# Kernel optimization log

Hardware: AMD Instinct MI355X
Metric: run time of the kernel (lower is better)

## Reference

```python
import jax, jax.numpy as jnp
import numpy as np

B, G = 256, 24
N = B * G
D_IN, HEADS, D_HEAD = 128, 8, 64  # out_channels = in_channels//2 = 64, concat=False
EFF = HEADS * D_HEAD
EPS = 1e-5
SCALE = float(np.sqrt(D_HEAD))

def _gelu(x):
    return jax.nn.gelu(x, approximate=False)

def _pff(x, w1, b1, w2, b2):
    # PositionwiseFeedForward, dropout=0 (eval)
    return _gelu(x @ w1.T + b1) @ w2.T + b2

def _graph_norm_global(x, w, b, ms):
    # GraphNorm called without batch -> single graph over all N nodes
    mean = jnp.mean(x, axis=0, keepdims=True)
    out = x - mean * ms
    var = jnp.mean(out * out, axis=0, keepdims=True)
    return w * out / jnp.sqrt(var + EPS) + b

def _graph_norm(x, w, b, ms, batch, nseg):
    cnt = jax.ops.segment_sum(jnp.ones((x.shape[0],), x.dtype), batch, nseg)[:, None]
    mean = jax.ops.segment_sum(x, batch, nseg) / cnt
    out = x - mean[batch] * ms
    var = jax.ops.segment_sum(out * out, batch, nseg) / cnt
    return w * out / jnp.sqrt(var + EPS)[batch] + b

def _segment_softmax(logits, seg, nseg):
    m = jax.ops.segment_max(logits, seg, num_segments=nseg)
    e = jnp.exp(logits - m[seg])
    s = jax.ops.segment_sum(e, seg, num_segments=nseg)
    return e / (s[seg] + 1e-16)

def _attn_conv(x, edge_index, p):
    (nq_w, nq_b, nq_ms, wq, bq, wk, bk, wv, bv,
     no_w, no_b, no_ms, o_w1, o_b1, o_w2, o_b2) = p
    n = x.shape[0]
    xin = x
    xn = _graph_norm_global(x, nq_w, nq_b, nq_ms)
    q = (xn @ wq.T + bq).reshape(n, HEADS, D_HEAD)
    k = (xn @ wk.T + bk).reshape(n, HEADS, D_HEAD)
    v = (xn @ wv.T + bv).reshape(n, HEADS, D_HEAD)
    loops = jnp.arange(n, dtype=edge_index.dtype)  # add_self_loops appends
    src = jnp.concatenate([edge_index[0], loops])
    dst = jnp.concatenate([edge_index[1], loops])
    qk = jnp.sum(q[dst] * k[src], axis=-1) / SCALE          # [E', H]
    alpha = _segment_softmax(qk, dst, n)                     # segment softmax over dst
    aggr = jax.ops.segment_sum(v[src] * alpha[:, :, None], dst, num_segments=n)  # [N,H,Dh]
    aggr = aggr.mean(axis=1)                                 # concat=False: head mean -> [N,64]
    init = xin.reshape(n, D_IN // D_HEAD, D_HEAD).sum(axis=1)  # sum-fold 128 -> 64 residual
    h = aggr + init
    hn = _graph_norm_global(h, no_w, no_b, no_ms)
    return h + _pff(hn, o_w1, o_b1, o_w2, o_b2)


def setup_inputs() -> dict:
    key = jax.random.key(0)
    ks = jax.random.split(key, 12)
    # block-dense edges: fully connected within each set, no self loops
    a = np.arange(G)
    ii, jj = np.meshgrid(a, a, indexing='ij')
    m = ii != jj
    dst_l, src_l = ii[m], jj[m]
    offs = (np.arange(B) * G)[:, None]
    src = (src_l[None, :] + offs).reshape(-1)
    dst = (dst_l[None, :] + offs).reshape(-1)
    edge_index = jnp.asarray(np.stack([src, dst]), dtype=jnp.int64)
    batch = jnp.asarray(np.repeat(np.arange(B), G), dtype=jnp.int64)
    ptr = jnp.asarray(np.arange(B + 1) * G, dtype=jnp.int64)
    x = jax.random.normal(ks[0], (N, D_IN), jnp.float32)
    def lin(k, o, i):
        return jax.random.normal(k, (o, i), jnp.float32) * (1.0 / np.sqrt(i))
    d = dict(x=x, edge_index=edge_index, ptr=ptr, batch=batch)
    d.update(nq_w=jnp.ones((D_IN,)), nq_b=jnp.zeros((D_IN,)), nq_ms=jnp.ones((D_IN,)))
    d.update(wq=lin(ks[1], EFF, D_IN), bq=jnp.zeros((EFF,)),
             wk=lin(ks[2], EFF, D_IN), bk=jnp.zeros((EFF,)),
             wv=lin(ks[3], EFF, D_IN), bv=jnp.zeros((EFF,)))
    d.update(no_w=jnp.ones((D_HEAD,)), no_b=jnp.zeros((D_HEAD,)), no_ms=jnp.ones((D_HEAD,)))
    d.update(o_w1=lin(ks[4], D_HEAD, D_HEAD), o_b1=jnp.zeros((D_HEAD,)),
             o_w2=lin(ks[5], D_HEAD, D_HEAD), o_b2=jnp.zeros((D_HEAD,)))
    d.update(pn_w=jnp.ones((D_HEAD,)), pn_b=jnp.zeros((D_HEAD,)), pn_ms=jnp.ones((D_HEAD,)))
    d.update(p_w1=lin(ks[6], D_HEAD, D_HEAD), p_b1=jnp.zeros((D_HEAD,)),
             p_w2=lin(ks[7], 1, D_HEAD), p_b2=jnp.zeros((1,)))
    return d


def reference(x, edge_index, ptr, batch,
              nq_w, nq_b, nq_ms, wq, bq, wk, bk, wv, bv,
              no_w, no_b, no_ms, o_w1, o_b1, o_w2, o_b2,
              pn_w, pn_b, pn_ms, p_w1, p_b1, p_w2, p_b2):
    nseg = ptr.shape[0] - 1
    h = _attn_conv(x, edge_index,
                   (nq_w, nq_b, nq_ms, wq, bq, wk, bk, wv, bv,
                    no_w, no_b, no_ms, o_w1, o_b1, o_w2, o_b2))   # [N,64]
    hn = _graph_norm(h, pn_w, pn_b, pn_ms, batch, nseg)
    score = _pff(hn, p_w1, p_b1, p_w2, p_b2)                       # [N,1]
    w = _segment_softmax(score[:, 0], batch, nseg)[:, None]        # per-set softmax
    return jax.ops.segment_sum(x * w, batch, num_segments=nseg)    # [B, 128]
```

## Files before the change

kernel.cpp:

```cpp
#include <hip/hip_runtime.h>
#include <stdint.h>


#define N_NODES 6144
#define GSIZE 24
#define NGRAPH 256
#define DIN 128
#define DH 64
#define EFF 512
#define EPSN 1e-5f

typedef __attribute__((ext_vector_type(8))) __bf16 bf16x8;
typedef __attribute__((ext_vector_type(4))) float f32x4;
union U16B { uint4 u; bf16x8 v; unsigned short s[8]; };

__device__ inline unsigned short f2bf(float f){
  unsigned u = __float_as_uint(f);
  u += 0x7fff + ((u>>16)&1);
  return (unsigned short)(u>>16);
}
__device__ inline float gelu_exact(float x){ return 0.5f*x*(1.0f+erff(x*0.70710678118654752f)); }

#define XS    0
#define HS    256
#define WT1   81920
#define WT2   86016
#define PWT1  90112
#define FBo   94208
#define WCVT_BYTE  385024
#define HCOMB_BYTE 778240

#define QSTRIDE 516

__global__ __launch_bounds__(256)
void k_pre(const float* __restrict__ x,
           const float* __restrict__ o_w1, const float* __restrict__ o_w2,
           const float* __restrict__ p_w1,
           const float* __restrict__ o_b1, const float* __restrict__ o_b2,
           const float* __restrict__ p_b1, const float* __restrict__ p_w2,
           const float* __restrict__ p_b2,
           const float* __restrict__ wq, const float* __restrict__ wk,
           const float* __restrict__ wv,
           float* __restrict__ wsf){
  int t = threadIdx.x;
  int bi = blockIdx.x;
  if(bi < 192){
    int c = t & 127, h = t >> 7;
    float s = 0.f, q = 0.f;
    #pragma unroll
    for(int r = 0; r < 16; ++r){
      float v = x[(size_t)(bi*32 + h + 2*r)*DIN + c];
      s += v; q += v*v;
    }
    __shared__ float sm[256], sm2[256];
    sm[t] = s; sm2[t] = q;
    __syncthreads();
    if(t < 128){
      atomicAdd(&wsf[XS + t],       sm[t] + sm[t+128]);
      atomicAdd(&wsf[XS + 128 + t], sm2[t] + sm2[t+128]);
    }
    return;
  }
  if(bi < 195){
    const float* src; float* dst;
    if(bi == 192){ src = o_w1; dst = wsf + WT1; }
    else if(bi == 193){ src = o_w2; dst = wsf + WT2; }
    else { src = p_w1; dst = wsf + PWT1; }
    for(int p = t; p < DH*DH; p += 256){
      int r = p >> 6, c = p & 63;
      dst[c*DH + r] = src[p];
    }
    if(bi == 192){
      float* fb = wsf + FBo;
      if(t < 64){
        fb[t]       = o_b1[t];
        fb[64 + t]  = o_b2[t];
        fb[128 + t] = p_b1[t];
        fb[192 + t] = p_w2[t];
      }
      if(t == 0) fb[256] = p_b2[0];
    }
    return;
  }
  int j = bi - 195;
  int mat = j >> 2, seg = j & 3;
  const float* src = (mat==0) ? wq : (mat==1) ? wk : wv;
  unsigned short* dst = (unsigned short*)((char*)wsf + WCVT_BYTE)
                        + (size_t)mat*EFF*DIN + seg*16384;
  const float* sp = src + seg*16384;
  for(int e = t*8; e < 16384; e += 2048){
    float4 a = *(const float4*)(sp + e);
    float4 b = *(const float4*)(sp + e + 4);
    U16B o;
    o.s[0]=f2bf(a.x); o.s[1]=f2bf(a.y); o.s[2]=f2bf(a.z); o.s[3]=f2bf(a.w);
    o.s[4]=f2bf(b.x); o.s[5]=f2bf(b.y); o.s[6]=f2bf(b.z); o.s[7]=f2bf(b.w);
    *(uint4*)(dst + e) = o.u;
  }
}

#define LOADW(nt, W, B) do{ \
  const int mat_ = (nt)>>2, sub_ = (nt)&3; \
  const unsigned short* wp_ = wcvt + (size_t)mat_*EFF*DIN \
      + (size_t)(h*64 + sub_*16 + m)*DIN + lq*8; \
  W[0] = *(const uint4*)(wp_);      W[1] = *(const uint4*)(wp_ + 32); \
  W[2] = *(const uint4*)(wp_ + 64); W[3] = *(const uint4*)(wp_ + 96); \
  const float* bias_ = (mat_==0) ? bq : (mat_==1) ? bk : bv; \
  B = *(const float4*)(bias_ + h*64 + sub_*16 + lq*4); \
}while(0)

#define COMPW(nt, W, B) do{ \
  const int mat_ = (nt)>>2, sub_ = (nt)&3; \
  f32x4 a0_ = {0.f,0.f,0.f,0.f}, a1_ = {0.f,0.f,0.f,0.f}; \
  U16B w8_; \
  w8_.u = W[0]; \
  a0_ = __builtin_amdgcn_mfma_f32_16x16x32_bf16(w8_.v, afr[0][0], a0_, 0, 0, 0); \
  a1_ = __builtin_amdgcn_mfma_f32_16x16x32_bf16(w8_.v, afr[1][0], a1_, 0, 0, 0); \
  w8_.u = W[1]; \
  a0_ = __builtin_amdgcn_mfma_f32_16x16x32_bf16(w8_.v, afr[0][1], a0_, 0, 0, 0); \
  a1_ = __builtin_amdgcn_mfma_f32_16x16x32_bf16(w8_.v, afr[1][1], a1_, 0, 0, 0); \
  w8_.u = W[2]; \
  a0_ = __builtin_amdgcn_mfma_f32_16x16x32_bf16(w8_.v, afr[0][2], a0_, 0, 0, 0); \
  a1_ = __builtin_amdgcn_mfma_f32_16x16x32_bf16(w8_.v, afr[1][2], a1_, 0, 0, 0); \
  w8_.u = W[3]; \
  a0_ = __builtin_amdgcn_mfma_f32_16x16x32_bf16(w8_.v, afr[0][3], a0_, 0, 0, 0); \
  a1_ = __builtin_amdgcn_mfma_f32_16x16x32_bf16(w8_.v, afr[1][3], a1_, 0, 0, 0); \
  float* dst_ = qlds + mat_*(GSIZE*QSTRIDE); \
  const int col_ = h*64 + sub_*16 + lq*4; \
  { float4 o_; o_.x=a0_[0]+B.x; o_.y=a0_[1]+B.y; o_.z=a0_[2]+B.z; o_.w=a0_[3]+B.w; \
    *(float4*)(dst_ + m*QSTRIDE + col_) = o_; } \
  if(m < 8){ float4 o_; o_.x=a1_[0]+B.x; o_.y=a1_[1]+B.y; o_.z=a1_[2]+B.z; o_.w=a1_[3]+B.w; \
    *(float4*)(dst_ + (16+m)*QSTRIDE + col_) = o_; } \
}while(0)

__global__ __launch_bounds__(512)
void k_attn2(const float* __restrict__ x,
             const float* __restrict__ bq, const float* __restrict__ bk,
             const float* __restrict__ bv,
             const float* __restrict__ nq_w, const float* __restrict__ nq_b,
             const float* __restrict__ nq_ms,
             float* __restrict__ ws, float* __restrict__ hcomb){
  __shared__ __align__(16) float qlds[3*GSIZE*QSTRIDE];
  __shared__ __align__(16) float hv[GSIZE][68];
  __shared__ float A1s[DIN], C1s[DIN];

  int t = threadIdx.x, g = blockIdx.x, base = g*GSIZE;
  int h = t >> 6, l = t & 63;
  const unsigned short* wcvt = (const unsigned short*)((const char*)ws + WCVT_BYTE);

  for(int i = t; i < GSIZE*68; i += 512) ((float*)hv)[i] = 0.f;

  if(t < 128){
    float s1 = ws[XS + t];
    float q1 = ws[XS + 128 + t];
    float mean = s1 * (1.0f / N_NODES);
    float ex2  = q1 * (1.0f / N_NODES);
    float cm   = mean * nq_ms[t];
    float var  = ex2 - 2.f*cm*mean + cm*cm;
    float rstd = rsqrtf(var + EPSN);
    float a    = nq_w[t] * rstd;
    A1s[t] = a; C1s[t] = nq_b[t] - a*cm;
  }
  __syncthreads();

  int m = l & 15, lq = l >> 4;

  bf16x8 afr[2][4];
  #pragma unroll
  for(int mt = 0; mt < 2; ++mt){
    int row = mt*16 + m; if(row > GSIZE-1) row = GSIZE-1;
    const float* xr = x + (size_t)(base + row)*DIN;
    #pragma unroll
    for(int kk = 0; kk < 4; ++kk){
      int k0 = kk*32 + lq*8;
      float4 a = *(const float4*)(xr + k0);
      float4 b = *(const float4*)(xr + k0 + 4);
      U16B u;
      u.s[0] = f2bf(a.x*A1s[k0+0] + C1s[k0+0]);
      u.s[1] = f2bf(a.y*A1s[k0+1] + C1s[k0+1]);
      u.s[2] = f2bf(a.z*A1s[k0+2] + C1s[k0+2]);
      u.s[3] = f2bf(a.w*A1s[k0+3] + C1s[k0+3]);
      u.s[4] = f2bf(b.x*A1s[k0+4] + C1s[k0+4]);
      u.s[5] = f2bf(b.y*A1s[k0+5] + C1s[k0+5]);
      u.s[6] = f2bf(b.z*A1s[k0+6] + C1s[k0+6]);
      u.s[7] = f2bf(b.w*A1s[k0+7] + C1s[k0+7]);
      afr[mt][kk] = u.v;
    }
  }

  {
    uint4 wA[4], wB[4], wC[4];
    float4 bA, bB, bC;
    LOADW(0, wA, bA);  LOADW(1, wB, bB);
    LOADW(2, wC, bC);  COMPW(0, wA, bA);
    LOADW(3, wA, bA);  COMPW(1, wB, bB);
    LOADW(4, wB, bB);  COMPW(2, wC, bC);
    LOADW(5, wC, bC);  COMPW(3, wA, bA);
    LOADW(6, wA, bA);  COMPW(4, wB, bB);
    LOADW(7, wB, bB);  COMPW(5, wC, bC);
    LOADW(8, wC, bC);  COMPW(6, wA, bA);
    LOADW(9, wA, bA);  COMPW(7, wB, bB);
    LOADW(10, wB, bB); COMPW(8, wC, bC);
    LOADW(11, wC, bC); COMPW(9, wA, bA);
    COMPW(10, wB, bB);
    COMPW(11, wC, bC);
  }

  float pr[3][3];
  {
    int r0 = 3*(l >> 3), j0 = 3*(l & 7);
    const float* qp = qlds + r0*QSTRIDE + h*64;
    const float* kp = qlds + GSIZE*QSTRIDE + j0*QSTRIDE + h*64;
    float s00=0.f,s01=0.f,s02=0.f,s10=0.f,s11=0.f,s12=0.f,s20=0.f,s21=0.f,s22=0.f;
    #pragma unroll
    for(int d4 = 0; d4 < 16; ++d4){
      float4 q0 = *(const float4*)(qp + d4*4);
      float4 q1 = *(const float4*)(qp + QSTRIDE + d4*4);
      float4 q2 = *(const float4*)(qp + 2*QSTRIDE + d4*4);
      float4 k0 = *(const float4*)(kp + d4*4);
      float4 k1 = *(const float4*)(kp + QSTRIDE + d4*4);
      float4 k2 = *(const float4*)(kp + 2*QSTRIDE + d4*4);
      s00 += q0.x*k0.x + q0.y*k0.y + q0.z*k0.z + q0.w*k0.w;
      s01 += q0.x*k1.x + q0.y*k1.y + q0.z*k1.z + q0.w*k1.w;
      s02 += q0.x*k2.x + q0.y*k2.y + q0.z*k2.z + q0.w*k2.w;
      s10 += q1.x*k0.x + q1.y*k0.y + q1.z*k0.z + q1.w*k0.w;
      s11 += q1.x*k1.x + q1.y*k1.y + q1.z*k1.z + q1.w*k1.w;
      s12 += q1.x*k2.x + q1.y*k2.y + q1.z*k2.z + q1.w*k2.w;
      s20 += q2.x*k0.x + q2.y*k0.y + q2.z*k0.z + q2.w*k0.w;
      s21 += q2.x*k1.x + q2.y*k1.y + q2.z*k1.z + q2.w*k1.w;
      s22 += q2.x*k2.x + q2.y*k2.y + q2.z*k2.z + q2.w*k2.w;
    }
    float a0, a1, a2, m0, su, inv;
    a0 = s00*0.125f; a1 = s01*0.125f; a2 = s02*0.125f;
    m0 = fmaxf(fmaxf(a0, a1), a2);
    #pragma unroll
    for(int o = 1; o < 8; o <<= 1) m0 = fmaxf(m0, __shfl_xor(m0, o, 8));
    a0 = __expf(a0-m0); a1 = __expf(a1-m0); a2 = __expf(a2-m0);
    su = a0 + a1 + a2;
    #pragma unroll
    for(int o = 1; o < 8; o <<= 1) su += __shfl_xor(su, o, 8);
    inv = 1.0f/(su + 1e-16f);
    pr[0][0] = a0*inv; pr[0][1] = a1*inv; pr[0][2] = a2*inv;
    a0 = s10*0.125f; a1 = s11*0.125f; a2 = s12*0.125f;
    m0 = fmaxf(fmaxf(a0, a1), a2);
    #pragma unroll
    for(int o = 1; o < 8; o <<= 1) m0 = fmaxf(m0, __shfl_xor(m0, o, 8));
    a0 = __expf(a0-m0); a1 = __expf(a1-m0); a2 = __expf(a2-m0);
    su = a0 + a1 + a2;
    #pragma unroll
    for(int o = 1; o < 8; o <<= 1) su += __shfl_xor(su, o, 8);
    inv = 1.0f/(su + 1e-16f);
    pr[1][0] = a0*inv; pr[1][1] = a1*inv; pr[1][2] = a2*inv;
    a0 = s20*0.125f; a1 = s21*0.125f; a2 = s22*0.125f;
    m0 = fmaxf(fmaxf(a0, a1), a2);
    #pragma unroll
    for(int o = 1; o < 8; o <<= 1) m0 = fmaxf(m0, __shfl_xor(m0, o, 8));
    a0 = __expf(a0-m0); a1 = __expf(a1-m0); a2 = __expf(a2-m0);
    su = a0 + a1 + a2;
    #pragma unroll
    for(int o = 1; o < 8; o <<= 1) su += __shfl_xor(su, o, 8);
    inv = 1.0f/(su + 1e-16f);
    pr[2][0] = a0*inv; pr[2][1] = a1*inv; pr[2][2] = a2*inv;
  }

  {
    float o24[GSIZE];
    #pragma unroll
    for(int r = 0; r < GSIZE; ++r) o24[r] = 0.f;
    const float* vp = qlds + 2*GSIZE*QSTRIDE + h*64 + l;
    #pragma unroll
    for(int j = 0; j < GSIZE; ++j){
      float v = vp[j*QSTRIDE];
      const int jg = j/3, jj = j%3;
      #pragma unroll
      for(int rg = 0; rg < 8; ++rg){
        #pragma unroll
        for(int rr = 0; rr < 3; ++rr){
          float pv = __uint_as_float(
              __builtin_amdgcn_readlane(__float_as_uint(pr[rr][jj]), rg*8 + jg));
          o24[rg*3+rr] = fmaf(pv, v, o24[rg*3+rr]);
        }
      }
    }
    #pragma unroll
    for(int r = 0; r < GSIZE; ++r) atomicAdd(&hv[r][l], o24[r]);
  }
  __syncthreads();

  #pragma unroll
  for(int sl = 0; sl < 3; ++sl){
    int idx = t + sl*512;
    int r = idx >> 6, d = idx & 63;
    const float* xr = x + (size_t)(base + r)*DIN;
    float hval = hv[r][d]*0.125f + xr[d] + xr[64 + d];
    hcomb[(size_t)(base + r)*DH + d] = hval;
    hv[r][d] = hval;
  }
  __syncthreads();
  if(t < 64){
    float s1 = 0.f, s2 = 0.f;
    #pragma unroll
    for(int i = 0; i < GSIZE; ++i){ float v = hv[i][t]; s1 += v; s2 += v*v; }
    atomicAdd(&ws[HS + t],      s1);
    atomicAdd(&ws[HS + 64 + t], s2);
  }
}

__global__ __launch_bounds__(512)
void k_final(const float* __restrict__ x,
             const float* __restrict__ hbuf, const float* __restrict__ ws,
             const float* __restrict__ no_w, const float* __restrict__ no_b,
             const float* __restrict__ no_ms,
             const float* __restrict__ pn_w, const float* __restrict__ pn_b,
             const float* __restrict__ pn_ms,
             float* __restrict__ out){
  __shared__ __align__(16) float W1[4096];
  __shared__ __align__(16) float W2[4096];
  __shared__ __align__(16) float PW1[4096];
  __shared__ __align__(16) float fbs[260];
  __shared__ __align__(16) float hs[GSIZE][68];
  __shared__ __align__(16) float hn[GSIZE][68];
  __shared__ __align__(16) float ts[GSIZE][68];
  __shared__ float A2s[DH], C2s[DH];
  __shared__ float a3[DH], c3[DH];
  __shared__ float scores[GSIZE], wsm[GSIZE];

  int t = threadIdx.x;
  int base = blockIdx.x * GSIZE;
  int c = t & 63, i0 = t >> 6;

  {
    const float4* s1 = (const float4*)(ws + WT1);
    const float4* s2 = (const float4*)(ws + WT2);
    const float4* s3 = (const float4*)(ws + PWT1);
    #pragma unroll
    for(int it = 0; it < 2; ++it){
      int i = t + it*512;
      ((float4*)W1)[i]  = s1[i];
      ((float4*)W2)[i]  = s2[i];
      ((float4*)PW1)[i] = s3[i];
    }
    if(t < 257) fbs[t] = ws[FBo + t];
    if(t < DH){
      float a1 = ws[HS + t];
      float a2 = ws[HS + 64 + t];
      float mean = a1 * (1.0f / N_NODES);
      float ex2  = a2 * (1.0f / N_NODES);
      float cm   = mean * no_ms[t];
      float var  = ex2 - 2.f*cm*mean + cm*cm;
      float rstd = rsqrtf(var + EPSN);
      float a    = no_w[t] * rstd;
      A2s[t] = a; C2s[t] = no_b[t] - a*cm;
    }
  }
  __syncthreads();
  {
    float a2 = A2s[c];
    float c2 = C2s[c];
    #pragma unroll
    for(int r = 0; r < 3; ++r){
      int i = i0 + 8*r;
      float hvv = hbuf[(size_t)(base + i)*DH + c];
      hs[i][c] = hvv;
      hn[i][c] = a2*hvv + c2;
    }
  }
  __syncthreads();

  {
    float acc[3];
    #pragma unroll
    for(int r = 0; r < 3; ++r) acc[r] = fbs[c];
    #pragma unroll 16
    for(int k = 0; k < DH; ++k){
      float w = W1[k*DH + c];
      #pragma unroll
      for(int r = 0; r < 3; ++r) acc[r] = fmaf(hn[i0 + 8*r][k], w, acc[r]);
    }
    #pragma unroll
    for(int r = 0; r < 3; ++r) ts[i0 + 8*r][c] = gelu_exact(acc[r]);
  }
  __syncthreads();

  {
    float acc[3];
    #pragma unroll
    for(int r = 0; r < 3; ++r) acc[r] = fbs[64 + c];
    #pragma unroll 16
    for(int k = 0; k < DH; ++k){
      float w = W2[k*DH + c];
      #pragma unroll
      for(int r = 0; r < 3; ++r) acc[r] = fmaf(ts[i0 + 8*r][k], w, acc[r]);
    }
    #pragma unroll
    for(int r = 0; r < 3; ++r) hs[i0 + 8*r][c] += acc[r];
  }
  __syncthreads();

  if(t < DH){
    float s1 = 0.f, s2 = 0.f;
    #pragma unroll
    for(int i = 0; i < GSIZE; i++){ float v = hs[i][t]; s1 += v; s2 += v*v; }
    float mean = s1 * (1.0f / GSIZE);
    float ex2  = s2 * (1.0f / GSIZE);
    float cm   = mean * pn_ms[t];
    float var  = ex2 - 2.f*cm*mean + cm*cm;
    float rstd = rsqrtf(var + EPSN);
    float a    = pn_w[t] * rstd;
    a3[t] = a; c3[t] = pn_b[t] - a*cm;
  }
  __syncthreads();

  {
    float acc[3];
    #pragma unroll
    for(int r = 0; r < 3; ++r) acc[r] = fbs[128 + c];
    #pragma unroll 16
    for(int k = 0; k < DH; ++k){
      float w  = PW1[k*DH + c];
      float ak = a3[k], ck = c3[k];
      #pragma unroll
      for(int r = 0; r < 3; ++r){
        float hnv = fmaf(ak, hs[i0 + 8*r][k], ck);
        acc[r] = fmaf(hnv, w, acc[r]);
      }
    }
    #pragma unroll
    for(int r = 0; r < 3; ++r) ts[i0 + 8*r][c] = gelu_exact(acc[r]);
  }
  __syncthreads();

  if(t < GSIZE){
    const float4* tp = (const float4*)ts[t];
    const float4* wp = (const float4*)(fbs + 192);
    float s = fbs[256];
    #pragma unroll
    for(int q = 0; q < 16; ++q){
      float4 a = tp[q], b = wp[q];
      s += a.x*b.x + a.y*b.y + a.z*b.z + a.w*b.w;
    }
    scores[t] = s;
  }
  __syncthreads();
  if(t < GSIZE){
    float mx = -1e30f;
    #pragma unroll
    for(int j = 0; j < GSIZE; j++) mx = fmaxf(mx, scores[j]);
    float sum = 0.f;
    #pragma unroll
    for(int j = 0; j < GSIZE; j++) sum += __expf(scores[j] - mx);
    wsm[t] = __expf(scores[t] - mx) / (sum + 1e-16f);
  }
  __syncthreads();
  if(t < DIN){
    float s = 0.f;
    #pragma unroll 8
    for(int i = 0; i < GSIZE; i++) s += wsm[i] * x[(size_t)(base+i)*DIN + t];
    out[(size_t)blockIdx.x*DIN + t] = s;
  }
}

extern "C" void kernel_launch(void* const* d_in, const int* in_sizes, int n_in,
                              void* d_out, int out_size, void* d_ws, size_t ws_size,
                              hipStream_t stream){
  (void)in_sizes; (void)n_in; (void)out_size; (void)ws_size;
  const float* x    = (const float*)d_in[0];
  const float* nq_w = (const float*)d_in[4];
  const float* nq_b = (const float*)d_in[5];
  const float* nq_ms= (const float*)d_in[6];
  const float* wq   = (const float*)d_in[7];
  const float* bq   = (const float*)d_in[8];
  const float* wk   = (const float*)d_in[9];
  const float* bk   = (const float*)d_in[10];
  const float* wv   = (const float*)d_in[11];
  const float* bv   = (const float*)d_in[12];
  const float* no_w = (const float*)d_in[13];
  const float* no_b = (const float*)d_in[14];
  const float* no_ms= (const float*)d_in[15];
  const float* o_w1 = (const float*)d_in[16];
  const float* o_b1 = (const float*)d_in[17];
  const float* o_w2 = (const float*)d_in[18];
  const float* o_b2 = (const float*)d_in[19];
  const float* pn_w = (const float*)d_in[20];
  const float* pn_b = (const float*)d_in[21];
  const float* pn_ms= (const float*)d_in[22];
  const float* p_w1 = (const float*)d_in[23];
  const float* p_b1 = (const float*)d_in[24];
  const float* p_w2 = (const float*)d_in[25];
  const float* p_b2 = (const float*)d_in[26];

  float* ws    = (float*)d_ws;
  float* hcomb = (float*)((char*)d_ws + HCOMB_BYTE);

  hipMemsetAsync(d_ws, 0, 384*sizeof(float), stream);
  k_pre<<<207, 256, 0, stream>>>(x, o_w1, o_w2, p_w1, o_b1, o_b2, p_b1, p_w2, p_b2,
                                 wq, wk, wv, ws);
  k_attn2<<<NGRAPH, 512, 0, stream>>>(x, bq, bk, bv, nq_w, nq_b, nq_ms, ws, hcomb);
  k_final<<<NGRAPH, 512, 0, stream>>>(x, hcomb, ws, no_w, no_b, no_ms,
                                      pn_w, pn_b, pn_ms, (float*)d_out);
}
```

Measured before the change: 166.3 us.

## Merge three kernels into one cooperative kernel with grid-wide syncs

Replaces the memset plus three separate launches (preprocess, attention, final) with a single cooperative kernel that uses grid.sync between phases. Global statistics go into per-block partial slots that every block reduces after the sync, so no atomics or memset are needed. The per-graph h values stay in shared memory across phases instead of going through a global buffer. The trade-offs are the cost of the grid barriers, the redundant partial reductions done by every block, and the constraint that all 256 blocks with about 156 KB of shared memory each must be co-resident.

```diff
diff --git a/kernel.cpp b/kernel.cpp
--- a/kernel.cpp
+++ b/kernel.cpp
@@ -1,5 +1,8 @@
 #include <hip/hip_runtime.h>
+#include <hip/hip_cooperative_groups.h>
 #include <stdint.h>
+
+namespace cg = cooperative_groups;
 
 
 #define N_NODES 6144
@@ -21,82 +24,24 @@
 }
 __device__ inline float gelu_exact(float x){ return 0.5f*x*(1.0f+erff(x*0.70710678118654752f)); }
 
-#define XS    0
-#define HS    256
-#define WT1   81920
-#define WT2   86016
-#define PWT1  90112
-#define FBo   94208
-#define WCVT_BYTE  385024
-#define HCOMB_BYTE 778240
+#define XP    0
+#define HP    65536
+#define WT1   98304
+#define WT2   102400
+#define PWT1  106496
+#define FBo   110592
+#define WCVT_BYTE 458752
 
 #define QSTRIDE 516
-
-__global__ __launch_bounds__(256)
-void k_pre(const float* __restrict__ x,
-           const float* __restrict__ o_w1, const float* __restrict__ o_w2,
-           const float* __restrict__ p_w1,
-           const float* __restrict__ o_b1, const float* __restrict__ o_b2,
-           const float* __restrict__ p_b1, const float* __restrict__ p_w2,
-           const float* __restrict__ p_b2,
-           const float* __restrict__ wq, const float* __restrict__ wk,
-           const float* __restrict__ wv,
-           float* __restrict__ wsf){
-  int t = threadIdx.x;
-  int bi = blockIdx.x;
-  if(bi < 192){
-    int c = t & 127, h = t >> 7;
-    float s = 0.f, q = 0.f;
-    #pragma unroll
-    for(int r = 0; r < 16; ++r){
-      float v = x[(size_t)(bi*32 + h + 2*r)*DIN + c];
-      s += v; q += v*v;
-    }
-    __shared__ float sm[256], sm2[256];
-    sm[t] = s; sm2[t] = q;
-    __syncthreads();
-    if(t < 128){
-      atomicAdd(&wsf[XS + t],       sm[t] + sm[t+128]);
-      atomicAdd(&wsf[XS + 128 + t], sm2[t] + sm2[t+128]);
-    }
-    return;
-  }
-  if(bi < 195){
-    const float* src; float* dst;
-    if(bi == 192){ src = o_w1; dst = wsf + WT1; }
-    else if(bi == 193){ src = o_w2; dst = wsf + WT2; }
-    else { src = p_w1; dst = wsf + PWT1; }
-    for(int p = t; p < DH*DH; p += 256){
-      int r = p >> 6, c = p & 63;
-      dst[c*DH + r] = src[p];
-    }
-    if(bi == 192){
-      float* fb = wsf + FBo;
-      if(t < 64){
-        fb[t]       = o_b1[t];
-        fb[64 + t]  = o_b2[t];
-        fb[128 + t] = p_b1[t];
-        fb[192 + t] = p_w2[t];
-      }
-      if(t == 0) fb[256] = p_b2[0];
-    }
-    return;
-  }
-  int j = bi - 195;
-  int mat = j >> 2, seg = j & 3;
-  const float* src = (mat==0) ? wq : (mat==1) ? wk : wv;
-  unsigned short* dst = (unsigned short*)((char*)wsf + WCVT_BYTE)
-                        + (size_t)mat*EFF*DIN + seg*16384;
-  const float* sp = src + seg*16384;
-  for(int e = t*8; e < 16384; e += 2048){
-    float4 a = *(const float4*)(sp + e);
-    float4 b = *(const float4*)(sp + e + 4);
-    U16B o;
-    o.s[0]=f2bf(a.x); o.s[1]=f2bf(a.y); o.s[2]=f2bf(a.z); o.s[3]=f2bf(a.w);
-    o.s[4]=f2bf(b.x); o.s[5]=f2bf(b.y); o.s[6]=f2bf(b.z); o.s[7]=f2bf(b.w);
-    *(uint4*)(dst + e) = o.u;
-  }
-}
+#define ARENA_HV 148608
+#define ARENA_A1 155136
+
+struct PP {
+  const float *x,*wq,*bq,*wk,*bk,*wv,*bv,*nq_w,*nq_b,*nq_ms,
+              *no_w,*no_b,*no_ms,*o_w1,*o_b1,*o_w2,*o_b2,
+              *pn_w,*pn_b,*pn_ms,*p_w1,*p_b1,*p_w2,*p_b2;
+  float *ws, *out;
+};
 
 #define LOADW(nt, W, B) do{ \
   const int mat_ = (nt)>>2, sub_ = (nt)&3; \
@@ -109,7 +54,6 @@
 }while(0)
 
 #define COMPW(nt, W, B) do{ \
-  const int mat_ = (nt)>>2, sub_ = (nt)&3; \
   f32x4 a0_ = {0.f,0.f,0.f,0.f}, a1_ = {0.f,0.f,0.f,0.f}; \
   U16B w8_; \
   w8_.u = W[0]; \
@@ -124,6 +68,7 @@
   w8_.u = W[3]; \
   a0_ = __builtin_amdgcn_mfma_f32_16x16x32_bf16(w8_.v, afr[0][3], a0_, 0, 0, 0); \
   a1_ = __builtin_amdgcn_mfma_f32_16x16x32_bf16(w8_.v, afr[1][3], a1_, 0, 0, 0); \
+  const int mat_ = (nt)>>2, sub_ = (nt)&3; \
   float* dst_ = qlds + mat_*(GSIZE*QSTRIDE); \
   const int col_ = h*64 + sub_*16 + lq*4; \
   { float4 o_; o_.x=a0_[0]+B.x; o_.y=a0_[1]+B.y; o_.z=a0_[2]+B.z; o_.w=a0_[3]+B.w; \
@@ -133,34 +78,92 @@
 }while(0)
 
 __global__ __launch_bounds__(512)
-void k_attn2(const float* __restrict__ x,
-             const float* __restrict__ bq, const float* __restrict__ bk,
-             const float* __restrict__ bv,
-             const float* __restrict__ nq_w, const float* __restrict__ nq_b,
-             const float* __restrict__ nq_ms,
-             float* __restrict__ ws, float* __restrict__ hcomb){
-  __shared__ __align__(16) float qlds[3*GSIZE*QSTRIDE];
-  __shared__ __align__(16) float hv[GSIZE][68];
-  __shared__ float A1s[DIN], C1s[DIN];
-
+void k_mega(PP p){
+  __shared__ __align__(16) char arena[156160];
+  float* ws = p.ws;
+  const float* x = p.x;
   int t = threadIdx.x, g = blockIdx.x, base = g*GSIZE;
+
+  {
+    int gidx = g*512 + t;
+    if(gidx < 24576){
+      int mat = gidx >> 13;
+      int off = (gidx & 8191) * 8;
+      const float* src = (mat==0) ? p.wq : (mat==1) ? p.wk : p.wv;
+      unsigned short* dst = (unsigned short*)((char*)ws + WCVT_BYTE)
+                            + (size_t)mat*EFF*DIN;
+      float4 a = *(const float4*)(src + off);
+      float4 b = *(const float4*)(src + off + 4);
+      U16B o;
+      o.s[0]=f2bf(a.x); o.s[1]=f2bf(a.y); o.s[2]=f2bf(a.z); o.s[3]=f2bf(a.w);
+      o.s[4]=f2bf(b.x); o.s[5]=f2bf(b.y); o.s[6]=f2bf(b.z); o.s[7]=f2bf(b.w);
+      *(uint4*)(dst + off) = o.u;
+    } else if(gidx < 36864){
+      int e = gidx - 24576;
+      int mat = e >> 12, q = e & 4095;
+      const float* src = (mat==0) ? p.o_w1 : (mat==1) ? p.o_w2 : p.p_w1;
+      float* dst = ws + ((mat==0) ? WT1 : (mat==1) ? WT2 : PWT1);
+      dst[(q & 63)*64 + (q >> 6)] = src[q];
+    } else if(gidx < 37121){
+      int e = gidx - 36864;
+      float v;
+      if(e < 64)       v = p.o_b1[e];
+      else if(e < 128) v = p.o_b2[e-64];
+      else if(e < 192) v = p.p_b1[e-128];
+      else if(e < 256) v = p.p_w2[e-192];
+      else             v = p.p_b2[0];
+      ws[FBo + e] = v;
+    }
+    float* smA = (float*)arena;
+    float* smB = smA + 512;
+    int c = t & 127, grp = t >> 7;
+    float s = 0.f, q2 = 0.f;
+    for(int r = grp*6; r < grp*6 + 6; ++r){
+      float v = x[(size_t)(base + r)*DIN + c];
+      s += v; q2 += v*v;
+    }
+    smA[t] = s; smB[t] = q2;
+    __syncthreads();
+    if(t < 128){
+      ws[XP + g*256 + t]       = smA[t] + smA[t+128] + smA[t+256] + smA[t+384];
+      ws[XP + g*256 + 128 + t] = smB[t] + smB[t+128] + smB[t+256] + smB[t+384];
+    }
+  }
+  cg::this_grid().sync();
+
+  float* qlds = (float*)arena;
+  float (*hv)[68] = (float(*)[68])(arena + ARENA_HV);
+  float* A1s = (float*)(arena + ARENA_A1);
+  float* C1s = A1s + 128;
+  const unsigned short* wcvt = (const unsigned short*)((const char*)ws + WCVT_BYTE);
+  const float *bq = p.bq, *bk = p.bk, *bv = p.bv;
   int h = t >> 6, l = t & 63;
-  const unsigned short* wcvt = (const unsigned short*)((const char*)ws + WCVT_BYTE);
 
   for(int i = t; i < GSIZE*68; i += 512) ((float*)hv)[i] = 0.f;
 
-  if(t < 128){
-    float s1 = ws[XS + t];
-    float q1 = ws[XS + 128 + t];
-    float mean = s1 * (1.0f / N_NODES);
-    float ex2  = q1 * (1.0f / N_NODES);
-    float cm   = mean * nq_ms[t];
-    float var  = ex2 - 2.f*cm*mean + cm*cm;
-    float rstd = rsqrtf(var + EPSN);
-    float a    = nq_w[t] * rstd;
-    A1s[t] = a; C1s[t] = nq_b[t] - a*cm;
-  }
-  __syncthreads();
+  {
+    float* redA = qlds; float* redB = qlds + 512;
+    int c = t & 127, grp = t >> 7;
+    float s = 0.f, q = 0.f;
+    for(int pp = grp*64; pp < grp*64 + 64; ++pp){
+      s += ws[XP + pp*256 + c];
+      q += ws[XP + pp*256 + 128 + c];
+    }
+    redA[t] = s; redB[t] = q;
+    __syncthreads();
+    if(t < 128){
+      float s1 = redA[t] + redA[t+128] + redA[t+256] + redA[t+384];
+      float q1 = redB[t] + redB[t+128] + redB[t+256] + redB[t+384];
+      float mean = s1 * (1.0f / N_NODES);
+      float ex2  = q1 * (1.0f / N_NODES);
+      float cm   = mean * p.nq_ms[t];
+      float var  = ex2 - 2.f*cm*mean + cm*cm;
+      float rstd = rsqrtf(var + EPSN);
+      float a    = p.nq_w[t] * rstd;
+      A1s[t] = a; C1s[t] = p.nq_b[t] - a*cm;
+    }
+    __syncthreads();
+  }
 
   int m = l & 15, lq = l >> 4;
 
@@ -291,171 +294,173 @@
     int idx = t + sl*512;
     int r = idx >> 6, d = idx & 63;
     const float* xr = x + (size_t)(base + r)*DIN;
-    float hval = hv[r][d]*0.125f + xr[d] + xr[64 + d];
-    hcomb[(size_t)(base + r)*DH + d] = hval;
-    hv[r][d] = hval;
+    hv[r][d] = hv[r][d]*0.125f + xr[d] + xr[64 + d];
   }
   __syncthreads();
   if(t < 64){
     float s1 = 0.f, s2 = 0.f;
     #pragma unroll
     for(int i = 0; i < GSIZE; ++i){ float v = hv[i][t]; s1 += v; s2 += v*v; }
-    atomicAdd(&ws[HS + t],      s1);
-    atomicAdd(&ws[HS + 64 + t], s2);
-  }
-}
-
-__global__ __launch_bounds__(512)
-void k_final(const float* __restrict__ x,
-             const float* __restrict__ hbuf, const float* __restrict__ ws,
-             const float* __restrict__ no_w, const float* __restrict__ no_b,
-             const float* __restrict__ no_ms,
-             const float* __restrict__ pn_w, const float* __restrict__ pn_b,
-             const float* __restrict__ pn_ms,
-             float* __restrict__ out){
-  __shared__ __align__(16) float W1[4096];
-  __shared__ __align__(16) float W2[4096];
-  __shared__ __align__(16) float PW1[4096];
-  __shared__ __align__(16) float fbs[260];
-  __shared__ __align__(16) float hs[GSIZE][68];
-  __shared__ __align__(16) float hn[GSIZE][68];
-  __shared__ __align__(16) float ts[GSIZE][68];
-  __shared__ float A2s[DH], C2s[DH];
-  __shared__ float a3[DH], c3[DH];
-  __shared__ float scores[GSIZE], wsm[GSIZE];
-
-  int t = threadIdx.x;
-  int base = blockIdx.x * GSIZE;
-  int c = t & 63, i0 = t >> 6;
+    ws[HP + g*128 + t]      = s1;
+    ws[HP + g*128 + 64 + t] = s2;
+  }
+  cg::this_grid().sync();
 
   {
-    const float4* s1 = (const float4*)(ws + WT1);
-    const float4* s2 = (const float4*)(ws + WT2);
-    const float4* s3 = (const float4*)(ws + PWT1);
-    #pragma unroll
-    for(int it = 0; it < 2; ++it){
-      int i = t + it*512;
-      ((float4*)W1)[i]  = s1[i];
-      ((float4*)W2)[i]  = s2[i];
-      ((float4*)PW1)[i] = s3[i];
-    }
-    if(t < 257) fbs[t] = ws[FBo + t];
+    float* W1  = (float*)arena;
+    float* W2  = (float*)(arena + 16384);
+    float* PW1 = (float*)(arena + 32768);
+    float* fbs = (float*)(arena + 49152);
+    float (*hs)[68] = (float(*)[68])(arena + ARENA_HV);
+    float (*hn)[68] = (float(*)[68])(arena + 50192);
+    float (*ts)[68] = (float(*)[68])(arena + 56720);
+    float* A2s = (float*)(arena + 63248);
+    float* C2s = (float*)(arena + 63504);
+    float* a3  = (float*)(arena + 63760);
+    float* c3  = (float*)(arena + 64016);
+    float* scores = (float*)(arena + 64272);
+    float* wsm = (float*)(arena + 64368);
+    float* redA = (float*)(arena + 64464);
+    float* redB = (float*)(arena + 66512);
+
+    int c = t & 63, i0 = t >> 6;
+
+    {
+      const float4* s1p = (const float4*)(ws + WT1);
+      const float4* s2p = (const float4*)(ws + WT2);
+      const float4* s3p = (const float4*)(ws + PWT1);
+      #pragma unroll
+      for(int it = 0; it < 2; ++it){
+        int i = t + it*512;
+        ((float4*)W1)[i]  = s1p[i];
+        ((float4*)W2)[i]  = s2p[i];
+        ((float4*)PW1)[i] = s3p[i];
+      }
+      if(t < 257) fbs[t] = ws[FBo + t];
+      int g8 = t >> 6;
+      float r1 = 0.f, r2 = 0.f;
+      for(int pp = g8*32; pp < g8*32 + 32; ++pp){
+        r1 += ws[HP + pp*128 + c];
+        r2 += ws[HP + pp*128 + 64 + c];
+      }
+      redA[t] = r1; redB[t] = r2;
+    }
+    __syncthreads();
     if(t < DH){
-      float a1 = ws[HS + t];
-      float a2 = ws[HS + 64 + t];
+      float a1 = redA[t]+redA[t+64]+redA[t+128]+redA[t+192]
+               + redA[t+256]+redA[t+320]+redA[t+384]+redA[t+448];
+      float a2 = redB[t]+redB[t+64]+redB[t+128]+redB[t+192]
+               + redB[t+256]+redB[t+320]+redB[t+384]+redB[t+448];
       float mean = a1 * (1.0f / N_NODES);
       float ex2  = a2 * (1.0f / N_NODES);
-      float cm   = mean * no_ms[t];
+      float cm   = mean * p.no_ms[t];
       float var  = ex2 - 2.f*cm*mean + cm*cm;
       float rstd = rsqrtf(var + EPSN);
-      float a    = no_w[t] * rstd;
-      A2s[t] = a; C2s[t] = no_b[t] - a*cm;
-    }
-  }
-  __syncthreads();
-  {
-    float a2 = A2s[c];
-    float c2 = C2s[c];
-    #pragma unroll
-    for(int r = 0; r < 3; ++r){
-      int i = i0 + 8*r;
-      float hvv = hbuf[(size_t)(base + i)*DH + c];
-      hs[i][c] = hvv;
-      hn[i][c] = a2*hvv + c2;
-    }
-  }
-  __syncthreads();
-
-  {
-    float acc[3];
-    #pragma unroll
-    for(int r = 0; r < 3; ++r) acc[r] = fbs[c];
-    #pragma unroll 16
-    for(int k = 0; k < DH; ++k){
-      float w = W1[k*DH + c];
-      #pragma unroll
-      for(int r = 0; r < 3; ++r) acc[r] = fmaf(hn[i0 + 8*r][k], w, acc[r]);
-    }
-    #pragma unroll
-    for(int r = 0; r < 3; ++r) ts[i0 + 8*r][c] = gelu_exact(acc[r]);
-  }
-  __syncthreads();
-
-  {
-    float acc[3];
-    #pragma unroll
-    for(int r = 0; r < 3; ++r) acc[r] = fbs[64 + c];
-    #pragma unroll 16
-    for(int k = 0; k < DH; ++k){
-      float w = W2[k*DH + c];
-      #pragma unroll
-      for(int r = 0; r < 3; ++r) acc[r] = fmaf(ts[i0 + 8*r][k], w, acc[r]);
-    }
-    #pragma unroll
-    for(int r = 0; r < 3; ++r) hs[i0 + 8*r][c] += acc[r];
-  }
-  __syncthreads();
-
-  if(t < DH){
-    float s1 = 0.f, s2 = 0.f;
-    #pragma unroll
-    for(int i = 0; i < GSIZE; i++){ float v = hs[i][t]; s1 += v; s2 += v*v; }
-    float mean = s1 * (1.0f / GSIZE);
-    float ex2  = s2 * (1.0f / GSIZE);
-    float cm   = mean * pn_ms[t];
-    float var  = ex2 - 2.f*cm*mean + cm*cm;
-    float rstd = rsqrtf(var + EPSN);
-    float a    = pn_w[t] * rstd;
-    a3[t] = a; c3[t] = pn_b[t] - a*cm;
-  }
-  __syncthreads();
-
-  {
-    float acc[3];
-    #pragma unroll
-    for(int r = 0; r < 3; ++r) acc[r] = fbs[128 + c];
-    #pragma unroll 16
-    for(int k = 0; k < DH; ++k){
-      float w  = PW1[k*DH + c];
-      float ak = a3[k], ck = c3[k];
+      float a    = p.no_w[t] * rstd;
+      A2s[t] = a; C2s[t] = p.no_b[t] - a*cm;
+    }
+    __syncthreads();
+    {
+      float a2 = A2s[c], c2v = C2s[c];
       #pragma unroll
       for(int r = 0; r < 3; ++r){
-        float hnv = fmaf(ak, hs[i0 + 8*r][k], ck);
-        acc[r] = fmaf(hnv, w, acc[r]);
-      }
-    }
-    #pragma unroll
-    for(int r = 0; r < 3; ++r) ts[i0 + 8*r][c] = gelu_exact(acc[r]);
-  }
-  __syncthreads();
-
-  if(t < GSIZE){
-    const float4* tp = (const float4*)ts[t];
-    const float4* wp = (const float4*)(fbs + 192);
-    float s = fbs[256];
-    #pragma unroll
-    for(int q = 0; q < 16; ++q){
-      float4 a = tp[q], b = wp[q];
-      s += a.x*b.x + a.y*b.y + a.z*b.z + a.w*b.w;
-    }
-    scores[t] = s;
-  }
-  __syncthreads();
-  if(t < GSIZE){
-    float mx = -1e30f;
-    #pragma unroll
-    for(int j = 0; j < GSIZE; j++) mx = fmaxf(mx, scores[j]);
-    float sum = 0.f;
-    #pragma unroll
-    for(int j = 0; j < GSIZE; j++) sum += __expf(scores[j] - mx);
-    wsm[t] = __expf(scores[t] - mx) / (sum + 1e-16f);
-  }
-  __syncthreads();
-  if(t < DIN){
-    float s = 0.f;
-    #pragma unroll 8
-    for(int i = 0; i < GSIZE; i++) s += wsm[i] * x[(size_t)(base+i)*DIN + t];
-    out[(size_t)blockIdx.x*DIN + t] = s;
+        int i = i0 + 8*r;
+        hn[i][c] = a2*hs[i][c] + c2v;
+      }
+    }
+    __syncthreads();
+
+    {
+      float acc[3];
+      #pragma unroll
+      for(int r = 0; r < 3; ++r) acc[r] = fbs[c];
+      #pragma unroll 16
+      for(int k = 0; k < DH; ++k){
+        float w = W1[k*DH + c];
+        #pragma unroll
+        for(int r = 0; r < 3; ++r) acc[r] = fmaf(hn[i0 + 8*r][k], w, acc[r]);
+      }
+      #pragma unroll
+      for(int r = 0; r < 3; ++r) ts[i0 + 8*r][c] = gelu_exact(acc[r]);
+    }
+    __syncthreads();
+
+    {
+      float acc[3];
+      #pragma unroll
+      for(int r = 0; r < 3; ++r) acc[r] = fbs[64 + c];
+      #pragma unroll 16
+      for(int k = 0; k < DH; ++k){
+        float w = W2[k*DH + c];
+        #pragma unroll
+        for(int r = 0; r < 3; ++r) acc[r] = fmaf(ts[i0 + 8*r][k], w, acc[r]);
+      }
+      #pragma unroll
+      for(int r = 0; r < 3; ++r) hs[i0 + 8*r][c] += acc[r];
+    }
+    __syncthreads();
+
+    if(t < DH){
+      float s1 = 0.f, s2 = 0.f;
+      #pragma unroll
+      for(int i = 0; i < GSIZE; i++){ float v = hs[i][t]; s1 += v; s2 += v*v; }
+      float mean = s1 * (1.0f / GSIZE);
+      float ex2  = s2 * (1.0f / GSIZE);
+      float cm   = mean * p.pn_ms[t];
+      float var  = ex2 - 2.f*cm*mean + cm*cm;
+      float rstd = rsqrtf(var + EPSN);
+      float a    = p.pn_w[t] * rstd;
+      a3[t] = a; c3[t] = p.pn_b[t] - a*cm;
+    }
+    __syncthreads();
+
+    {
+      float acc[3];
+      #pragma unroll
+      for(int r = 0; r < 3; ++r) acc[r] = fbs[128 + c];
+      #pragma unroll 16
+      for(int k = 0; k < DH; ++k){
+        float w  = PW1[k*DH + c];
+        float ak = a3[k], ck = c3[k];
+        #pragma unroll
+        for(int r = 0; r < 3; ++r){
+          float hnv = fmaf(ak, hs[i0 + 8*r][k], ck);
+          acc[r] = fmaf(hnv, w, acc[r]);
+        }
+      }
+      #pragma unroll
+      for(int r = 0; r < 3; ++r) ts[i0 + 8*r][c] = gelu_exact(acc[r]);
+    }
+    __syncthreads();
+
+    if(t < GSIZE){
+      const float4* tp = (const float4*)ts[t];
+      const float4* wp = (const float4*)(fbs + 192);
+      float s = fbs[256];
+      #pragma unroll
+      for(int q = 0; q < 16; ++q){
+        float4 a = tp[q], b = wp[q];
+        s += a.x*b.x + a.y*b.y + a.z*b.z + a.w*b.w;
+      }
+      scores[t] = s;
+    }
+    __syncthreads();
+    if(t < GSIZE){
+      float mx = -1e30f;
+      #pragma unroll
+      for(int j = 0; j < GSIZE; j++) mx = fmaxf(mx, scores[j]);
+      float sum = 0.f;
+      #pragma unroll
+      for(int j = 0; j < GSIZE; j++) sum += __expf(scores[j] - mx);
+      wsm[t] = __expf(scores[t] - mx) / (sum + 1e-16f);
+    }
+    __syncthreads();
+    if(t < DIN){
+      float s = 0.f;
+      #pragma unroll 8
+      for(int i = 0; i < GSIZE; i++) s += wsm[i] * x[(size_t)(base+i)*DIN + t];
+      p.out[(size_t)g*DIN + t] = s;
+    }
   }
 }
 
@@ -463,38 +468,35 @@
                               void* d_out, int out_size, void* d_ws, size_t ws_size,
                               hipStream_t stream){
   (void)in_sizes; (void)n_in; (void)out_size; (void)ws_size;
-  const float* x    = (const float*)d_in[0];
-  const float* nq_w = (const float*)d_in[4];
-  const float* nq_b = (const float*)d_in[5];
-  const float* nq_ms= (const float*)d_in[6];
-  const float* wq   = (const float*)d_in[7];
-  const float* bq   = (const float*)d_in[8];
-  const float* wk   = (const float*)d_in[9];
-  const float* bk   = (const float*)d_in[10];
-  const float* wv   = (const float*)d_in[11];
-  const float* bv   = (const float*)d_in[12];
-  const float* no_w = (const float*)d_in[13];
-  const float* no_b = (const float*)d_in[14];
-  const float* no_ms= (const float*)d_in[15];
-  const float* o_w1 = (const float*)d_in[16];
-  const float* o_b1 = (const float*)d_in[17];
-  const float* o_w2 = (const float*)d_in[18];
-  const float* o_b2 = (const float*)d_in[19];
-  const float* pn_w = (const float*)d_in[20];
-  const float* pn_b = (const float*)d_in[21];
-  const float* pn_ms= (const float*)d_in[22];
-  const float* p_w1 = (const float*)d_in[23];
-  const float* p_b1 = (const float*)d_in[24];
-  const float* p_w2 = (const float*)d_in[25];
-  const float* p_b2 = (const float*)d_in[26];
-
-  float* ws    = (float*)d_ws;
-  float* hcomb = (float*)((char*)d_ws + HCOMB_BYTE);
-
-  hipMemsetAsync(d_ws, 0, 384*sizeof(float), stream);
-  k_pre<<<207, 256, 0, stream>>>(x, o_w1, o_w2, p_w1, o_b1, o_b2, p_b1, p_w2, p_b2,
-                                 wq, wk, wv, ws);
-  k_attn2<<<NGRAPH, 512, 0, stream>>>(x, bq, bk, bv, nq_w, nq_b, nq_ms, ws, hcomb);
-  k_final<<<NGRAPH, 512, 0, stream>>>(x, hcomb, ws, no_w, no_b, no_ms,
-                                      pn_w, pn_b, pn_ms, (float*)d_out);
+  PP prm;
+  prm.x    = (const float*)d_in[0];
+  prm.nq_w = (const float*)d_in[4];
+  prm.nq_b = (const float*)d_in[5];
+  prm.nq_ms= (const float*)d_in[6];
+  prm.wq   = (const float*)d_in[7];
+  prm.bq   = (const float*)d_in[8];
+  prm.wk   = (const float*)d_in[9];
+  prm.bk   = (const float*)d_in[10];
+  prm.wv   = (const float*)d_in[11];
+  prm.bv   = (const float*)d_in[12];
+  prm.no_w = (const float*)d_in[13];
+  prm.no_b = (const float*)d_in[14];
+  prm.no_ms= (const float*)d_in[15];
+  prm.o_w1 = (const float*)d_in[16];
+  prm.o_b1 = (const float*)d_in[17];
+  prm.o_w2 = (const float*)d_in[18];
+  prm.o_b2 = (const float*)d_in[19];
+  prm.pn_w = (const float*)d_in[20];
+  prm.pn_b = (const float*)d_in[21];
+  prm.pn_ms= (const float*)d_in[22];
+  prm.p_w1 = (const float*)d_in[23];
+  prm.p_b1 = (const float*)d_in[24];
+  prm.p_w2 = (const float*)d_in[25];
+  prm.p_b2 = (const float*)d_in[26];
+  prm.ws   = (float*)d_ws;
+  prm.out  = (float*)d_out;
+
+  void* kargs[] = { &prm };
+  hipLaunchCooperativeKernel((const void*)k_mega, dim3(NGRAPH), dim3(512),
+                             kargs, 0, stream);
 }
```

After: 260.9 us. +56.9%, slower.
